# Optimization experiments

Hardware: AMD Instinct MI355X
Metric: run time of the kernel (lower is better)

## Reference

```python
import jax, jax.numpy as jnp
import numpy as np

N = 131072   # total nodes
G = 4096     # graphs
E = 524288   # directed bond edges
C = 96       # hidden_channels
L = 8        # num_layers
F_IN = 64    # atom features
NT = 5       # targets


def setup_inputs() -> dict:
    key = jax.random.key(0)
    ks = jax.random.split(key, 32)
    def rn(k, shape, s=0.05):
        return jax.random.normal(k, shape, jnp.float32) * s
    inp = {
        'x': jax.random.normal(ks[0], (N, F_IN), jnp.float32),
        'edge_index': jax.random.randint(ks[1], (2, E), 0, N),
        'batch': jnp.sort(jax.random.randint(ks[2], (N,), 0, G)),
        'num_graphs': G,
        # atom encoder
        'enc_w': rn(ks[3], (F_IN, C)), 'enc_b': rn(ks[4], (C,)),
        # virtual node embedding + MLP (Linear->BN->SiLU->Linear)
        'vn_emb': rn(ks[5], (C,)),
        'vn_w1': rn(ks[6], (C, C)), 'vn_b1': rn(ks[7], (C,)),
        'vn_g1': 1.0 + rn(ks[8], (C,)), 'vn_be1': rn(ks[9], (C,)),
        'vn_w2': rn(ks[10], (C, C)), 'vn_b2': rn(ks[11], (C,)),
        # per-layer GIN MLP (Linear C->2C, BN, SiLU, Linear 2C->C) stacked over L
        'conv_w1': rn(ks[12], (L, C, 2 * C)), 'conv_b1': rn(ks[13], (L, 2 * C)),
        'conv_g1': 1.0 + rn(ks[14], (L, 2 * C)), 'conv_be1': rn(ks[15], (L, 2 * C)),
        'conv_w2': rn(ks[16], (L, 2 * C, C)), 'conv_b2': rn(ks[17], (L, C)),
        # per-layer outer BatchNorm
        'bn_g': 1.0 + rn(ks[18], (L, C)), 'bn_b': rn(ks[19], (L, C)),
        # head: C->C/2 (BN,SiLU) -> C/4 (BN,SiLU) -> NT
        'h_w1': rn(ks[20], (C, C // 2)), 'h_b1': rn(ks[21], (C // 2,)),
        'h_g1': 1.0 + rn(ks[22], (C // 2,)), 'h_be1': rn(ks[23], (C // 2,)),
        'h_w2': rn(ks[24], (C // 2, C // 4)), 'h_b2': rn(ks[25], (C // 4,)),
        'h_g2': 1.0 + rn(ks[26], (C // 4,)), 'h_be2': rn(ks[27], (C // 4,)),
        'h_w3': rn(ks[28], (C // 4, NT)), 'h_b3': rn(ks[29], (NT,)),
    }
    return inp


def _bn(x, g, b, eps=1e-5):
    # training-mode BatchNorm1d: biased batch variance (matches torch normalization)
    m = x.mean(0)
    v = x.var(0)
    return (x - m) * jax.lax.rsqrt(v + eps) * g + b


def reference(x, edge_index, batch, num_graphs, enc_w, enc_b, vn_emb,
              vn_w1, vn_b1, vn_g1, vn_be1, vn_w2, vn_b2,
              conv_w1, conv_b1, conv_g1, conv_be1, conv_w2, conv_b2,
              bn_g, bn_b,
              h_w1, h_b1, h_g1, h_be1, h_w2, h_b2, h_g2, h_be2, h_w3, h_b3):
    n = x.shape[0]
    gN = int(num_graphs)
    c = enc_w.shape[1]
    nl = conv_w1.shape[0]

    h = x @ enc_w + enc_b                                   # [n, C]
    vn = jnp.broadcast_to(vn_emb, (gN, c))                  # virtual node feats
    h = jnp.concatenate([h, vn], 0)                         # [n+gN, C]

    # vectorized virtual-node edges: (n+batch[i]) <-> i, both directions
    node_ids = jnp.arange(n, dtype=batch.dtype)
    vidx = n + batch
    src = jnp.concatenate([edge_index[0], vidx, node_ids])
    tgt = jnp.concatenate([edge_index[1], node_ids, vidx])
    total = n + gN

    for i in range(nl):
        # GINConv, eps=0: MLP(x + sum_neighbors)
        agg = jax.ops.segment_sum(h[src], tgt, num_segments=total)
        z = h + agg
        z = z @ conv_w1[i] + conv_b1[i]
        z = jax.nn.silu(_bn(z, conv_g1[i], conv_be1[i]))
        z = z @ conv_w2[i] + conv_b2[i]
        z = jax.nn.silu(_bn(z, bn_g[i], bn_b[i]))           # outer BN + SiLU (dropout=eval)
        h = z if i == 0 else h + z                          # residual after layer 0
        if i < nl - 1:
            v = h[n:]
            v = jax.nn.silu(_bn(v @ vn_w1 + vn_b1, vn_g1, vn_be1)) @ vn_w2 + vn_b2
            h = jnp.concatenate([h[:n], v], 0)

    hn = h[:n]
    sums = jax.ops.segment_sum(hn, batch, num_segments=gN)
    counts = jax.ops.segment_sum(jnp.ones((n,), hn.dtype), batch, num_segments=gN)
    pooled = sums / jnp.maximum(counts, 1.0)[:, None]       # global_mean_pool

    z = jax.nn.silu(_bn(pooled @ h_w1 + h_b1, h_g1, h_be1))
    z = jax.nn.silu(_bn(z @ h_w2 + h_b2, h_g2, h_be2))
    return z @ h_w3 + h_b3                                  # [G, 5]
```

## Files before the change

kernel.cpp:

```cpp
#include <hip/hip_runtime.h>
#include <hip/hip_bf16.h>

constexpr int N_   = 131072;
constexpr int G_   = 4096;
constexpr int E_   = 524288;
constexpr int C_   = 96;
constexpr int L_   = 8;
constexpr int FIN_ = 64;
constexpr int TOT_ = N_ + G_;

typedef __attribute__((ext_vector_type(8))) short short8v;
typedef __attribute__((ext_vector_type(4))) float f32x4;
using bf16 = __hip_bfloat16;

__device__ __forceinline__ float silu_f(float y) { return y / (1.f + __expf(-y)); }
__device__ __forceinline__ float toF(float x) { return x; }
__device__ __forceinline__ float toF(bf16 x)  { return __bfloat162float(x); }
__device__ __forceinline__ float bfbits2f(short s) {
  return __uint_as_float(((unsigned)(unsigned short)s) << 16);
}
__device__ __forceinline__ short f2bfbits(float f) {
  bf16 b = __float2bfloat16(f);
  return *reinterpret_cast<short*>(&b);
}
__device__ __forceinline__ void atomAddD(double* p, double v) { unsafeAtomicAdd(p, v); }

static inline int gblk(long n) { return (int)((n + 255) / 256); }

__global__ __launch_bounds__(256) void k_prep(const float* __restrict__ enc_w,
    const float* __restrict__ conv_w1, const float* __restrict__ conv_w2,
    const float* __restrict__ vn_w1, const float* __restrict__ vn_w2,
    bf16* __restrict__ encwT, bf16* __restrict__ w1T, bf16* __restrict__ w2T,
    bf16* __restrict__ vnw1T, bf16* __restrict__ vnw2T) {
  int idx = blockIdx.x * 256 + threadIdx.x;
  const float* src; bf16* dst; int Kd, Nd, local;
  if (idx < 6144)        { src = enc_w;   dst = encwT; Kd = 64;  Nd = 96;  local = idx; }
  else if (idx < 153600) { src = conv_w1; dst = w1T;   Kd = 96;  Nd = 192; local = idx - 6144; }
  else if (idx < 301056) { src = conv_w2; dst = w2T;   Kd = 192; Nd = 96;  local = idx - 153600; }
  else if (idx < 310272) { src = vn_w1;   dst = vnw1T; Kd = 96;  Nd = 96;  local = idx - 301056; }
  else if (idx < 319488) { src = vn_w2;   dst = vnw2T; Kd = 96;  Nd = 96;  local = idx - 310272; }
  else return;
  int per = Kd * Nd;
  int i   = local / per;
  int rem = local - i * per;
  int k   = rem / Nd;
  int n   = rem - k * Nd;
  dst[(size_t)i * per + n * Kd + k] = __float2bfloat16(src[local]);
}

__global__ __launch_bounds__(256) void k_deg_count(const int* __restrict__ tgt, int* __restrict__ deg) {
  int e = blockIdx.x * 256 + threadIdx.x;
  if (e >= E_) return;
  atomicAdd(&deg[tgt[e]], 1);
}

__global__ __launch_bounds__(256) void k_scan_local(const int* __restrict__ deg, int* __restrict__ lp,
                                                    int* __restrict__ bsum) {
  __shared__ int s[256];
  int t = threadIdx.x;
  int i = blockIdx.x * 256 + t;
  int v = deg[i];
  s[t] = v;
  __syncthreads();
  for (int off = 1; off < 256; off <<= 1) {
    int x = (t >= off) ? s[t - off] : 0;
    __syncthreads();
    s[t] += x;
    __syncthreads();
  }
  lp[i] = s[t] - v;
  if (t == 255) bsum[blockIdx.x] = s[255];
}

__global__ __launch_bounds__(512) void k_scan_bsum(const int* __restrict__ bsum, int* __restrict__ boff) {
  __shared__ int s[512];
  int t = threadIdx.x;
  int v = bsum[t];
  s[t] = v;
  __syncthreads();
  for (int off = 1; off < 512; off <<= 1) {
    int x = (t >= off) ? s[t - off] : 0;
    __syncthreads();
    s[t] += x;
    __syncthreads();
  }
  boff[t] = s[t] - v;
}

__global__ __launch_bounds__(256) void k_scan_add(int* __restrict__ rs, const int* __restrict__ boff) {
  int i = blockIdx.x * 256 + threadIdx.x;
  if (i > N_) return;
  if (i == N_) { rs[N_] = E_; return; }
  rs[i] += boff[i >> 8];
}

__global__ __launch_bounds__(256) void k_csr_fill(const int* __restrict__ src, const int* __restrict__ tgt,
                                                  const int* __restrict__ rs, int* __restrict__ cur,
                                                  int* __restrict__ ssrc) {
  int e = blockIdx.x * 256 + threadIdx.x;
  if (e >= E_) return;
  int t = tgt[e];
  int pos = atomicAdd(&cur[t], 1);
  ssrc[rs[t] + pos] = src[e];
}

__global__ __launch_bounds__(256) void k_gbounds(const int* __restrict__ batch, int* __restrict__ gstart) {
  int i = blockIdx.x * 256 + threadIdx.x;
  if (i > N_) return;
  if (i == N_) {
    int last = batch[N_ - 1];
    for (int g = last + 1; g <= G_; ++g) gstart[g] = N_;
    return;
  }
  int b  = batch[i];
  int bp = (i == 0) ? -1 : batch[i - 1];
  for (int g = bp + 1; g <= b; ++g) gstart[g] = i;
}

__global__ __launch_bounds__(192) void k_vnagg(const bf16* __restrict__ hb, const int* __restrict__ gstart,
                                               bf16* __restrict__ vna) {
  int slot = threadIdx.x / 24;
  int c4   = (threadIdx.x % 24) * 4;
  int g = blockIdx.x * 8 + slot;
  int i0 = gstart[g], i1 = gstart[g + 1];
  float s0 = 0.f, s1 = 0.f, s2 = 0.f, s3 = 0.f;
  for (int i = i0; i < i1; ++i) {
    short4 v = *(const short4*)((const short*)hb + (size_t)i * C_ + c4);
    s0 += bfbits2f(v.x); s1 += bfbits2f(v.y); s2 += bfbits2f(v.z); s3 += bfbits2f(v.w);
  }
  short4 o;
  o.x = f2bfbits(s0); o.y = f2bfbits(s1); o.z = f2bfbits(s2); o.w = f2bfbits(s3);
  *(short4*)((short*)vna + (size_t)g * C_ + c4) = o;
}

template <int K, int NOUT, bool INACT, bool OSTATS, bool AF32, bool NTA, bool NTO, typename OutT>
__global__ __launch_bounds__(512) void k_gemm(const void* __restrict__ Aptr, const bf16* __restrict__ Wt,
                                              const float* __restrict__ bias,
                                              const double* __restrict__ stin,
                                              const float* __restrict__ gam, const float* __restrict__ bet,
                                              float Rin,
                                              OutT* __restrict__ out, double* __restrict__ stout) {
  constexpr int KK  = K / 32;
  constexpr int NT  = NOUT / 16;
  constexpr int UPR = K / 8;
  constexpr int LPR = UPR + 1;
  constexpr int LWB  = NOUT * LPR * 16;
  constexpr int ISCB = INACT ? 2 * K * 4 : 0;
  constexpr int SMB  = LWB + (ISCB > 0 ? ISCB : 1);
  __shared__ __align__(16) char smem[SMB];
  uint4* lw   = reinterpret_cast<uint4*>(smem);
  float* lsc  = reinterpret_cast<float*>(smem + LWB);
  float* lsh  = lsc + K;
  float* ssum = reinterpret_cast<float*>(smem);
  float* sqs  = ssum + 8 * NOUT;

  const uint4* wv = (const uint4*)Wt;
  for (int u = threadIdx.x; u < NOUT * UPR; u += 512) {
    int row = u / UPR, colu = u - row * UPR;
    lw[row * LPR + colu] = wv[u];
  }
  if (INACT) {
    for (int k = threadIdx.x; k < K; k += 512) {
      double mean = stin[k] / (double)Rin;
      double var  = stin[K + k] / (double)Rin - mean * mean;
      float sc = gam[k] * rsqrtf((float)var + 1e-5f);
      lsc[k] = sc;
      lsh[k] = bet[k] - (float)mean * sc;
    }
  }

  int wave = threadIdx.x >> 6, lane = threadIdx.x & 63;
  int m0 = (blockIdx.x * 8 + wave) * 16;
  int lr = lane & 15, lg = lane >> 4;

  short8v a[KK];
  if constexpr (AF32) {
    const float* Arow = (const float*)Aptr + (size_t)(m0 + lr) * K + lg * 8;
#pragma unroll
    for (int kk = 0; kk < KK; ++kk) {
      float4 f0 = *(const float4*)(Arow + kk * 32);
      float4 f1 = *(const float4*)(Arow + kk * 32 + 4);
      a[kk][0] = f2bfbits(f0.x); a[kk][1] = f2bfbits(f0.y);
      a[kk][2] = f2bfbits(f0.z); a[kk][3] = f2bfbits(f0.w);
      a[kk][4] = f2bfbits(f1.x); a[kk][5] = f2bfbits(f1.y);
      a[kk][6] = f2bfbits(f1.z); a[kk][7] = f2bfbits(f1.w);
    }
  } else {
    const short* Arow = (const short*)Aptr + (size_t)(m0 + lr) * K + lg * 8;
#pragma unroll
    for (int kk = 0; kk < KK; ++kk) {
      if constexpr (NTA) a[kk] = __builtin_nontemporal_load((const short8v*)(Arow + kk * 32));
      else               a[kk] = *(const short8v*)(Arow + kk * 32);
    }
  }

  __syncthreads();

  if (INACT) {
#pragma unroll
    for (int kk = 0; kk < KK; ++kk) {
      int kbase = kk * 32 + lg * 8;
#pragma unroll
      for (int j = 0; j < 8; ++j) {
        float f = bfbits2f(a[kk][j]);
        f = silu_f(fmaf(f, lsc[kbase + j], lsh[kbase + j]));
        a[kk][j] = f2bfbits(f);
      }
    }
  }

  f32x4 acc[NT];
#pragma unroll
  for (int nt = 0; nt < NT; ++nt) acc[nt] = (f32x4){0.f, 0.f, 0.f, 0.f};

#pragma unroll
  for (int nt = 0; nt < NT; ++nt) {
    const short* brow = (const short*)&lw[(nt * 16 + lr) * LPR] + lg * 8;
#pragma unroll
    for (int kk = 0; kk < KK; ++kk) {
      short8v b = *(const short8v*)(brow + kk * 32);
      acc[nt] = __builtin_amdgcn_mfma_f32_16x16x32_bf16(a[kk], b, acc[nt], 0, 0, 0);
    }
  }

  if (OSTATS) __syncthreads();

  int orow = m0 + (lg << 2);
#pragma unroll
  for (int nt = 0; nt < NT; ++nt) {
    int col = nt * 16 + lr;
    float bi = bias[col];
    float s = 0.f, q = 0.f;
#pragma unroll
    for (int r = 0; r < 4; ++r) {
      float y = acc[nt][r] + bi;
      float yb;
      size_t off = (size_t)(orow + r) * NOUT + col;
      if constexpr (sizeof(OutT) == 2) {
        short bits = f2bfbits(y);
        if constexpr (NTO) __builtin_nontemporal_store(bits, (short*)out + off);
        else               ((short*)out)[off] = bits;
        yb = bfbits2f(bits);
      } else {
        if constexpr (NTO) __builtin_nontemporal_store(y, (float*)out + off);
        else               ((float*)out)[off] = y;
        yb = y;
      }
      if (OSTATS) { s += yb; q += yb * yb; }
    }
    if (OSTATS) {
      s += __shfl_xor(s, 16, 64); s += __shfl_xor(s, 32, 64);
      q += __shfl_xor(q, 16, 64); q += __shfl_xor(q, 32, 64);
      if (lg == 0) { ssum[wave * NOUT + col] = s; sqs[wave * NOUT + col] = q; }
    }
  }
  if (OSTATS) {
    __syncthreads();
    int tid = threadIdx.x;
    if (tid < NOUT) {
      float s = 0.f, q = 0.f;
#pragma unroll
      for (int w = 0; w < 8; ++w) { s += ssum[w * NOUT + tid]; q += sqs[w * NOUT + tid]; }
      atomAddD(&stout[tid], (double)s);
      atomAddD(&stout[NOUT + tid], (double)q);
    }
  }
}

template <int K, int NOUT>
__global__ __launch_bounds__(512) void k_gemm_agg(const bf16* __restrict__ hb,
    const int* __restrict__ batch, const int* __restrict__ rs, const int* __restrict__ ssrc,
    const bf16* __restrict__ vna, const bf16* __restrict__ Wt, const float* __restrict__ bias,
    bf16* __restrict__ out, double* __restrict__ st) {
  constexpr int KK  = K / 32;
  constexpr int NT  = NOUT / 16;
  constexpr int UPR = K / 8;
  constexpr int LPR = UPR + 1;
  constexpr int LWB = NOUT * LPR * 16;
  __shared__ __align__(16) char smem[LWB];
  uint4* lw   = reinterpret_cast<uint4*>(smem);
  float* ssum = reinterpret_cast<float*>(smem);
  float* sqs  = ssum + 8 * NOUT;

  const uint4* wv = (const uint4*)Wt;
  for (int u = threadIdx.x; u < NOUT * UPR; u += 512) {
    int row = u / UPR, colu = u - row * UPR;
    lw[row * LPR + colu] = wv[u];
  }

  int wave = threadIdx.x >> 6, lane = threadIdx.x & 63;
  int m0 = (blockIdx.x * 8 + wave) * 16;
  int lr = lane & 15, lg = lane >> 4;
  int row = m0 + lr;
  int koff = lg * 8;

  float av[KK * 8];
#pragma unroll
  for (int t = 0; t < KK * 8; ++t) av[t] = 0.f;

  auto addPtr = [&](const short* p) {
#pragma unroll
    for (int kk = 0; kk < KK; ++kk) {
      short8v v = *(const short8v*)(p + koff + kk * 32);
#pragma unroll
      for (int j = 0; j < 8; ++j) av[kk * 8 + j] += bfbits2f(v[j]);
    }
  };
  auto addPtr2 = [&](const short* p0, const short* p1) {
    short8v v0[KK], v1[KK];
#pragma unroll
    for (int kk = 0; kk < KK; ++kk) {
      v0[kk] = *(const short8v*)(p0 + koff + kk * 32);
      v1[kk] = *(const short8v*)(p1 + koff + kk * 32);
    }
#pragma unroll
    for (int kk = 0; kk < KK; ++kk)
#pragma unroll
      for (int j = 0; j < 8; ++j)
        av[kk * 8 + j] += bfbits2f(v0[kk][j]) + bfbits2f(v1[kk][j]);
  };
  auto hrow = [&](int r) { return (const short*)hb + (size_t)r * K; };

  if (row < N_) {
    addPtr2(hrow(row), hrow(N_ + batch[row]));
    int e = rs[row], e1 = rs[row + 1];
    for (; e + 2 <= e1; e += 2) addPtr2(hrow(ssrc[e]), hrow(ssrc[e + 1]));
    if (e < e1) addPtr(hrow(ssrc[e]));
  } else {
    addPtr2(hrow(row), (const short*)vna + (size_t)(row - N_) * K);
  }

  short8v a[KK];
#pragma unroll
  for (int kk = 0; kk < KK; ++kk)
#pragma unroll
    for (int j = 0; j < 8; ++j) a[kk][j] = f2bfbits(av[kk * 8 + j]);

  __syncthreads();

  f32x4 acc[NT];
#pragma unroll
  for (int nt = 0; nt < NT; ++nt) acc[nt] = (f32x4){0.f, 0.f, 0.f, 0.f};

#pragma unroll
  for (int nt = 0; nt < NT; ++nt) {
    const short* brow = (const short*)&lw[(nt * 16 + lr) * LPR] + lg * 8;
#pragma unroll
    for (int kk = 0; kk < KK; ++kk) {
      short8v b = *(const short8v*)(brow + kk * 32);
      acc[nt] = __builtin_amdgcn_mfma_f32_16x16x32_bf16(a[kk], b, acc[nt], 0, 0, 0);
    }
  }

  __syncthreads();

  int orow = m0 + (lg << 2);
#pragma unroll
  for (int nt = 0; nt < NT; ++nt) {
    int col = nt * 16 + lr;
    float bi = bias[col];
    float s = 0.f, q = 0.f;
#pragma unroll
    for (int r = 0; r < 4; ++r) {
      float y = acc[nt][r] + bi;
      short bits = f2bfbits(y);
      __builtin_nontemporal_store(bits, (short*)out + (size_t)(orow + r) * NOUT + col);
      float yb = bfbits2f(bits);
      s += yb; q += yb * yb;
    }
    s += __shfl_xor(s, 16, 64); s += __shfl_xor(s, 32, 64);
    q += __shfl_xor(q, 16, 64); q += __shfl_xor(q, 32, 64);
    if (lg == 0) { ssum[wave * NOUT + col] = s; sqs[wave * NOUT + col] = q; }
  }
  __syncthreads();
  int tid = threadIdx.x;
  if (tid < NOUT) {
    float s = 0.f, q = 0.f;
#pragma unroll
    for (int w = 0; w < 8; ++w) { s += ssum[w * NOUT + tid]; q += sqs[w * NOUT + tid]; }
    atomAddD(&st[tid], (double)s);
    atomAddD(&st[NOUT + tid], (double)q);
  }
}

__global__ __launch_bounds__(256) void k_fill_vn(bf16* __restrict__ hb, const float* __restrict__ vn) {
  int idx = blockIdx.x * 256 + threadIdx.x;
  if (idx >= G_ * C_) return;
  int c = idx % C_;
  hb[(size_t)N_ * C_ + idx] = __float2bfloat16(vn[c]);
}

template <int CC, typename T>
__global__ __launch_bounds__(256) void k_bnstats(const T* __restrict__ X, int R, double* __restrict__ st) {
  int c = threadIdx.x;
  float s = 0.f, q = 0.f;
  for (int r = blockIdx.x; r < R; r += gridDim.x) {
    float v = toF(X[(size_t)r * CC + c]);
    s += v;
    q += v * v;
  }
  atomAddD(&st[c], (double)s);
  atomAddD(&st[CC + c], (double)q);
}

template <int CC>
__global__ __launch_bounds__(256) void k_bnfin(const double* __restrict__ st, int R,
    const float* __restrict__ g, const float* __restrict__ be,
    float* __restrict__ scale, float* __restrict__ shift) {
  int c = threadIdx.x;
  if (c >= CC) return;
  double mean = st[c] / R;
  double var  = st[CC + c] / R - mean * mean;
  float sc = g[c] * rsqrtf((float)var + 1e-5f);
  scale[c] = sc;
  shift[c] = be[c] - (float)mean * sc;
}

__global__ __launch_bounds__(256) void k_update(const bf16* __restrict__ Z, bf16* __restrict__ hb,
    const double* __restrict__ st,
    const float* __restrict__ gam, const float* __restrict__ bet, int addResid) {
  __shared__ float lsc[C_], lsh[C_];
  if (threadIdx.x < C_) {
    int c = threadIdx.x;
    double mean = st[c] / (double)TOT_;
    double var  = st[C_ + c] / (double)TOT_ - mean * mean;
    float sc = gam[c] * rsqrtf((float)var + 1e-5f);
    lsc[c] = sc;
    lsh[c] = bet[c] - (float)mean * sc;
  }
  __syncthreads();
  int idx = blockIdx.x * 256 + threadIdx.x;
  if (idx >= TOT_ * C_ / 8) return;
  int cg = idx % (C_ / 8);
  int c0 = cg * 8;
  short8v zv = __builtin_nontemporal_load((const short8v*)Z + idx);
  short8v hv = ((const short8v*)hb)[idx];
  short8v o;
#pragma unroll
  for (int j = 0; j < 8; ++j) {
    float y = silu_f(fmaf(bfbits2f(zv[j]), lsc[c0 + j], lsh[c0 + j]));
    float hn = addResid ? (bfbits2f(hv[j]) + y) : y;
    o[j] = f2bfbits(hn);
  }
  ((short8v*)hb)[idx] = o;
}

template <int K, int M, bool INACT>
__global__ __launch_bounds__(256) void k_mm(const float* __restrict__ A,
    const float* __restrict__ W, const float* __restrict__ bias,
    const float* __restrict__ isc, const float* __restrict__ ish,
    float* __restrict__ out, int R) {
  int idx = blockIdx.x * 256 + threadIdx.x;
  if (idx >= R * M) return;
  int row = idx / M;
  int m   = idx - row * M;
  const float* ar = A + (size_t)row * K;
  float s = bias[m];
#pragma unroll 8
  for (int k = 0; k < K; ++k) {
    float a = ar[k];
    if (INACT) a = silu_f(fmaf(a, isc[k], ish[k]));
    s = fmaf(a, W[k * M + m], s);
  }
  out[idx] = s;
}

__global__ __launch_bounds__(256) void k_pool2(const bf16* __restrict__ hb, const int* __restrict__ gstart,
                                               float* __restrict__ pooled) {
  int idx = blockIdx.x * 256 + threadIdx.x;
  if (idx >= G_ * C_) return;
  int g = idx / C_;
  int c = idx - g * C_;
  int i0 = gstart[g], i1 = gstart[g + 1];
  float s = 0.f;
  for (int i = i0; i < i1; ++i) s += toF(hb[(size_t)i * C_ + c]);
  pooled[idx] = s / fmaxf((float)(i1 - i0), 1.0f);
}

extern "C" void kernel_launch(void* const* d_in, const int* in_sizes, int n_in,
                              void* d_out, int out_size, void* d_ws, size_t ws_size,
                              hipStream_t stream) {
  (void)in_sizes; (void)n_in; (void)out_size; (void)ws_size;
  const float* x       = (const float*)d_in[0];
  const int*   ei      = (const int*)d_in[1];
  const int*   batch   = (const int*)d_in[2];
  const float* enc_w   = (const float*)d_in[4];
  const float* enc_b   = (const float*)d_in[5];
  const float* vn_emb  = (const float*)d_in[6];
  const float* vn_w1   = (const float*)d_in[7];
  const float* vn_b1   = (const float*)d_in[8];
  const float* vn_g1   = (const float*)d_in[9];
  const float* vn_be1  = (const float*)d_in[10];
  const float* vn_w2   = (const float*)d_in[11];
  const float* vn_b2   = (const float*)d_in[12];
  const float* conv_w1 = (const float*)d_in[13];
  const float* conv_b1 = (const float*)d_in[14];
  const float* conv_g1 = (const float*)d_in[15];
  const float* conv_be1= (const float*)d_in[16];
  const float* conv_w2 = (const float*)d_in[17];
  const float* conv_b2 = (const float*)d_in[18];
  const float* bn_g    = (const float*)d_in[19];
  const float* bn_b    = (const float*)d_in[20];
  const float* h_w1    = (const float*)d_in[21];
  const float* h_b1    = (const float*)d_in[22];
  const float* h_g1    = (const float*)d_in[23];
  const float* h_be1   = (const float*)d_in[24];
  const float* h_w2    = (const float*)d_in[25];
  const float* h_b2    = (const float*)d_in[26];
  const float* h_g2    = (const float*)d_in[27];
  const float* h_be2   = (const float*)d_in[28];
  const float* h_w3    = (const float*)d_in[29];
  const float* h_b3    = (const float*)d_in[30];
  float* out = (float*)d_out;

  const int* e_src = ei;
  const int* e_tgt = ei + E_;

  char* p = (char*)d_ws;
  auto alloc = [&](size_t bytes) -> char* {
    char* r = p;
    p += (bytes + 15) & ~size_t(15);
    return r;
  };
  bf16*   hbf    = (bf16*)  alloc((size_t)TOT_ * C_ * 2);
  bf16*   vna    = (bf16*)  alloc((size_t)G_ * C_ * 2);
  bf16*   vtb    = (bf16*)  alloc((size_t)G_ * C_ * 2);
  float*  pooled = (float*) alloc((size_t)G_ * C_ * 4);
  float*  t1     = (float*) alloc((size_t)G_ * 48 * 4);
  float*  t2     = (float*) alloc((size_t)G_ * 24 * 4);
  float*  scale1 = (float*) alloc(256 * 4);
  float*  shift1 = (float*) alloc(256 * 4);
  float*  scale2 = (float*) alloc(256 * 4);
  float*  shift2 = (float*) alloc(256 * 4);
  double* stbuf  = (double*)alloc((size_t)26 * 384 * 8);
  bf16*   z1     = (bf16*)  alloc((size_t)TOT_ * 2 * C_ * 2);
  bf16*   z2     = (bf16*)  alloc((size_t)TOT_ * C_ * 2);
  bf16*   encwT  = (bf16*)  alloc((size_t)C_ * FIN_ * 2);
  bf16*   w1T    = (bf16*)  alloc((size_t)L_ * 2 * C_ * C_ * 2);
  bf16*   w2T    = (bf16*)  alloc((size_t)L_ * C_ * 2 * C_ * 2);
  bf16*   vnw1T  = (bf16*)  alloc((size_t)C_ * C_ * 2);
  bf16*   vnw2T  = (bf16*)  alloc((size_t)C_ * C_ * 2);
  int*    deg    = (int*)   alloc((size_t)N_ * 4);
  int*    cur    = (int*)   alloc((size_t)N_ * 4);
  int*    rs     = (int*)   alloc((size_t)(N_ + 1) * 4);
  int*    bsum   = (int*)   alloc(512 * 4);
  int*    boff   = (int*)   alloc(512 * 4);
  int*    ssrc   = (int*)   alloc((size_t)E_ * 4);
  int*    gstart = (int*)   alloc((size_t)(G_ + 1) * 4);

  auto ST = [&](int i) { return stbuf + (size_t)i * 384; };

  k_prep<<<gblk(319488), 256, 0, stream>>>(enc_w, conv_w1, conv_w2, vn_w1, vn_w2,
                                           encwT, w1T, w2T, vnw1T, vnw2T);

  hipMemsetAsync(deg, 0, (size_t)N_ * 4, stream);
  hipMemsetAsync(cur, 0, (size_t)N_ * 4, stream);
  hipMemsetAsync(stbuf, 0, (size_t)26 * 384 * 8, stream);
  k_deg_count<<<gblk(E_), 256, 0, stream>>>(e_tgt, deg);
  k_scan_local<<<N_ / 256, 256, 0, stream>>>(deg, rs, bsum);
  k_scan_bsum<<<1, 512, 0, stream>>>(bsum, boff);
  k_scan_add<<<gblk(N_ + 1), 256, 0, stream>>>(rs, boff);
  k_csr_fill<<<gblk(E_), 256, 0, stream>>>(e_src, e_tgt, rs, cur, ssrc);
  k_gbounds<<<gblk(N_ + 1), 256, 0, stream>>>(batch, gstart);

  k_gemm<FIN_, C_, false, false, true, false, false, bf16><<<N_ / 128, 512, 0, stream>>>(
      x, encwT, enc_b, nullptr, nullptr, nullptr, 1.f, hbf, nullptr);
  k_fill_vn<<<gblk((long)G_ * C_), 256, 0, stream>>>(hbf, vn_emb);

  for (int i = 0; i < L_; ++i) {
    const bf16*  wt1 = w1T + (size_t)i * 2 * C_ * C_;
    const bf16*  wt2 = w2T + (size_t)i * C_ * 2 * C_;
    const float* b1  = conv_b1 + (size_t)i * 2 * C_;
    const float* g1  = conv_g1 + (size_t)i * 2 * C_;
    const float* be1 = conv_be1+ (size_t)i * 2 * C_;
    const float* b2  = conv_b2 + (size_t)i * C_;
    const float* bg  = bn_g    + (size_t)i * C_;
    const float* bb  = bn_b    + (size_t)i * C_;

    k_vnagg<<<G_ / 8, 192, 0, stream>>>(hbf, gstart, vna);

    k_gemm_agg<C_, 2 * C_><<<TOT_ / 128, 512, 0, stream>>>(
        hbf, batch, rs, ssrc, vna, wt1, b1, z1, ST(i));

    k_gemm<2 * C_, C_, true, true, false, true, true, bf16><<<TOT_ / 128, 512, 0, stream>>>(
        z1, wt2, b2, ST(i), g1, be1, (float)TOT_, z2, ST(8 + i));

    k_update<<<(int)((long)TOT_ * C_ / 8 / 256), 256, 0, stream>>>(z2, hbf, ST(8 + i), bg, bb, i > 0);

    if (i < L_ - 1) {
      k_gemm<C_, C_, false, true, false, false, false, bf16><<<G_ / 128, 512, 0, stream>>>(
          hbf + (size_t)N_ * C_, vnw1T, vn_b1, nullptr, nullptr, nullptr, 1.f, vtb, ST(16 + i));
      k_gemm<C_, C_, true, false, false, false, false, bf16><<<G_ / 128, 512, 0, stream>>>(
          vtb, vnw2T, vn_b2, ST(16 + i), vn_g1, vn_be1, (float)G_,
          hbf + (size_t)N_ * C_, nullptr);
    }
  }

  k_pool2<<<gblk((long)G_ * C_), 256, 0, stream>>>(hbf, gstart, pooled);

  k_mm<C_, 48, false><<<gblk((long)G_ * 48), 256, 0, stream>>>(
      pooled, h_w1, h_b1, nullptr, nullptr, t1, G_);
  k_bnstats<48, float><<<64, 48, 0, stream>>>(t1, G_, ST(23));
  k_bnfin<48><<<1, 48, 0, stream>>>(ST(23), G_, h_g1, h_be1, scale1, shift1);

  k_mm<48, 24, true><<<gblk((long)G_ * 24), 256, 0, stream>>>(
      t1, h_w2, h_b2, scale1, shift1, t2, G_);
  k_bnstats<24, float><<<64, 24, 0, stream>>>(t2, G_, ST(24));
  k_bnfin<24><<<1, 24, 0, stream>>>(ST(24), G_, h_g2, h_be2, scale2, shift2);

  k_mm<24, 5, true><<<gblk((long)G_ * 5), 256, 0, stream>>>(
      t2, h_w3, h_b3, scale2, shift2, out, G_);
}
```

Before: 1.440 ms.

## Sort nodes by degree for load-balanced aggregation; drop nontemporal loads/stores

Builds a degree-bucketed permutation of nodes (histogram, prefix base, scatter) once per call, and has the aggregation+GEMM kernel process rows in that order so lanes within a wave walk similar neighbor counts, reducing divergence. Output rows are scattered back through the permutation via shuffled row ids. Also removes the nontemporal load/store variants from the GEMM, aggregation and update kernels so these intermediates can stay in cache. The price is extra setup kernels, an indirection per row, and scattered output writes.

```diff
diff --git a/kernel.cpp b/kernel.cpp
--- a/kernel.cpp
+++ b/kernel.cpp
@@ -117,6 +117,29 @@
   for (int g = bp + 1; g <= b; ++g) gstart[g] = i;
 }
 
+__global__ __launch_bounds__(256) void k_deghist(const int* __restrict__ deg, int* __restrict__ hist) {
+  int i = blockIdx.x * 256 + threadIdx.x;
+  if (i >= N_) return;
+  int b = deg[i]; if (b > 32) b = 32;
+  atomicAdd(&hist[b], 1);
+}
+
+__global__ __launch_bounds__(64) void k_degbase(const int* __restrict__ hist, int* __restrict__ base) {
+  if (threadIdx.x == 0) {
+    int acc = 0;
+    for (int b = 0; b < 33; ++b) { base[b] = acc; acc += hist[b]; }
+  }
+}
+
+__global__ __launch_bounds__(256) void k_permfill(const int* __restrict__ deg, const int* __restrict__ base,
+                                                  int* __restrict__ curs, int* __restrict__ perm) {
+  int i = blockIdx.x * 256 + threadIdx.x;
+  if (i >= N_) return;
+  int b = deg[i]; if (b > 32) b = 32;
+  int pos = atomicAdd(&curs[b], 1);
+  perm[base[b] + pos] = i;
+}
+
 __global__ __launch_bounds__(192) void k_vnagg(const bf16* __restrict__ hb, const int* __restrict__ gstart,
                                                bf16* __restrict__ vna) {
   int slot = threadIdx.x / 24;
@@ -133,7 +156,7 @@
   *(short4*)((short*)vna + (size_t)g * C_ + c4) = o;
 }
 
-template <int K, int NOUT, bool INACT, bool OSTATS, bool AF32, bool NTA, bool NTO, typename OutT>
+template <int K, int NOUT, bool INACT, bool OSTATS, bool AF32, typename OutT>
 __global__ __launch_bounds__(512) void k_gemm(const void* __restrict__ Aptr, const bf16* __restrict__ Wt,
                                               const float* __restrict__ bias,
                                               const double* __restrict__ stin,
@@ -188,10 +211,7 @@
   } else {
     const short* Arow = (const short*)Aptr + (size_t)(m0 + lr) * K + lg * 8;
 #pragma unroll
-    for (int kk = 0; kk < KK; ++kk) {
-      if constexpr (NTA) a[kk] = __builtin_nontemporal_load((const short8v*)(Arow + kk * 32));
-      else               a[kk] = *(const short8v*)(Arow + kk * 32);
-    }
+    for (int kk = 0; kk < KK; ++kk) a[kk] = *(const short8v*)(Arow + kk * 32);
   }
 
   __syncthreads();
@@ -238,12 +258,10 @@
       size_t off = (size_t)(orow + r) * NOUT + col;
       if constexpr (sizeof(OutT) == 2) {
         short bits = f2bfbits(y);
-        if constexpr (NTO) __builtin_nontemporal_store(bits, (short*)out + off);
-        else               ((short*)out)[off] = bits;
+        ((short*)out)[off] = bits;
         yb = bfbits2f(bits);
       } else {
-        if constexpr (NTO) __builtin_nontemporal_store(y, (float*)out + off);
-        else               ((float*)out)[off] = y;
+        ((float*)out)[off] = y;
         yb = y;
       }
       if (OSTATS) { s += yb; q += yb * yb; }
@@ -270,7 +288,8 @@
 template <int K, int NOUT>
 __global__ __launch_bounds__(512) void k_gemm_agg(const bf16* __restrict__ hb,
     const int* __restrict__ batch, const int* __restrict__ rs, const int* __restrict__ ssrc,
-    const bf16* __restrict__ vna, const bf16* __restrict__ Wt, const float* __restrict__ bias,
+    const bf16* __restrict__ vna, const int* __restrict__ perm,
+    const bf16* __restrict__ Wt, const float* __restrict__ bias,
     bf16* __restrict__ out, double* __restrict__ st) {
   constexpr int KK  = K / 32;
   constexpr int NT  = NOUT / 16;
@@ -292,6 +311,7 @@
   int m0 = (blockIdx.x * 8 + wave) * 16;
   int lr = lane & 15, lg = lane >> 4;
   int row = m0 + lr;
+  int rowo = (m0 < N_) ? perm[row] : row;
   int koff = lg * 8;
 
   float av[KK * 8];
@@ -321,13 +341,13 @@
   };
   auto hrow = [&](int r) { return (const short*)hb + (size_t)r * K; };
 
-  if (row < N_) {
-    addPtr2(hrow(row), hrow(N_ + batch[row]));
-    int e = rs[row], e1 = rs[row + 1];
+  if (m0 < N_) {
+    addPtr2(hrow(rowo), hrow(N_ + batch[rowo]));
+    int e = rs[rowo], e1 = rs[rowo + 1];
     for (; e + 2 <= e1; e += 2) addPtr2(hrow(ssrc[e]), hrow(ssrc[e + 1]));
     if (e < e1) addPtr(hrow(ssrc[e]));
   } else {
-    addPtr2(hrow(row), (const short*)vna + (size_t)(row - N_) * K);
+    addPtr2(hrow(rowo), (const short*)vna + (size_t)(rowo - N_) * K);
   }
 
   short8v a[KK];
@@ -354,7 +374,10 @@
 
   __syncthreads();
 
-  int orow = m0 + (lg << 2);
+  int rid[4];
+#pragma unroll
+  for (int r = 0; r < 4; ++r) rid[r] = __shfl(rowo, (lg << 2) + r, 64);
+
 #pragma unroll
   for (int nt = 0; nt < NT; ++nt) {
     int col = nt * 16 + lr;
@@ -364,7 +387,7 @@
     for (int r = 0; r < 4; ++r) {
       float y = acc[nt][r] + bi;
       short bits = f2bfbits(y);
-      __builtin_nontemporal_store(bits, (short*)out + (size_t)(orow + r) * NOUT + col);
+      ((short*)out)[(size_t)rid[r] * NOUT + col] = bits;
       float yb = bfbits2f(bits);
       s += yb; q += yb * yb;
     }
@@ -433,7 +456,7 @@
   if (idx >= TOT_ * C_ / 8) return;
   int cg = idx % (C_ / 8);
   int c0 = cg * 8;
-  short8v zv = __builtin_nontemporal_load((const short8v*)Z + idx);
+  short8v zv = ((const short8v*)Z)[idx];
   short8v hv = ((const short8v*)hb)[idx];
   short8v o;
 #pragma unroll
@@ -547,6 +570,10 @@
   int*    boff   = (int*)   alloc(512 * 4);
   int*    ssrc   = (int*)   alloc((size_t)E_ * 4);
   int*    gstart = (int*)   alloc((size_t)(G_ + 1) * 4);
+  int*    perm   = (int*)   alloc((size_t)N_ * 4);
+  int*    hist   = (int*)   alloc(33 * 4);
+  int*    hbase  = (int*)   alloc(33 * 4);
+  int*    hcurs  = (int*)   alloc(33 * 4);
 
   auto ST = [&](int i) { return stbuf + (size_t)i * 384; };
 
@@ -556,14 +583,19 @@
   hipMemsetAsync(deg, 0, (size_t)N_ * 4, stream);
   hipMemsetAsync(cur, 0, (size_t)N_ * 4, stream);
   hipMemsetAsync(stbuf, 0, (size_t)26 * 384 * 8, stream);
+  hipMemsetAsync(hist, 0, 33 * 4, stream);
+  hipMemsetAsync(hcurs, 0, 33 * 4, stream);
   k_deg_count<<<gblk(E_), 256, 0, stream>>>(e_tgt, deg);
   k_scan_local<<<N_ / 256, 256, 0, stream>>>(deg, rs, bsum);
   k_scan_bsum<<<1, 512, 0, stream>>>(bsum, boff);
   k_scan_add<<<gblk(N_ + 1), 256, 0, stream>>>(rs, boff);
   k_csr_fill<<<gblk(E_), 256, 0, stream>>>(e_src, e_tgt, rs, cur, ssrc);
   k_gbounds<<<gblk(N_ + 1), 256, 0, stream>>>(batch, gstart);
-
-  k_gemm<FIN_, C_, false, false, true, false, false, bf16><<<N_ / 128, 512, 0, stream>>>(
+  k_deghist<<<gblk(N_), 256, 0, stream>>>(deg, hist);
+  k_degbase<<<1, 64, 0, stream>>>(hist, hbase);
+  k_permfill<<<gblk(N_), 256, 0, stream>>>(deg, hbase, hcurs, perm);
+
+  k_gemm<FIN_, C_, false, false, true, bf16><<<N_ / 128, 512, 0, stream>>>(
       x, encwT, enc_b, nullptr, nullptr, nullptr, 1.f, hbf, nullptr);
   k_fill_vn<<<gblk((long)G_ * C_), 256, 0, stream>>>(hbf, vn_emb);
 
@@ -580,17 +612,17 @@
     k_vnagg<<<G_ / 8, 192, 0, stream>>>(hbf, gstart, vna);
 
     k_gemm_agg<C_, 2 * C_><<<TOT_ / 128, 512, 0, stream>>>(
-        hbf, batch, rs, ssrc, vna, wt1, b1, z1, ST(i));
-
-    k_gemm<2 * C_, C_, true, true, false, true, true, bf16><<<TOT_ / 128, 512, 0, stream>>>(
+        hbf, batch, rs, ssrc, vna, perm, wt1, b1, z1, ST(i));
+
+    k_gemm<2 * C_, C_, true, true, false, bf16><<<TOT_ / 128, 512, 0, stream>>>(
         z1, wt2, b2, ST(i), g1, be1, (float)TOT_, z2, ST(8 + i));
 
     k_update<<<(int)((long)TOT_ * C_ / 8 / 256), 256, 0, stream>>>(z2, hbf, ST(8 + i), bg, bb, i > 0);
 
     if (i < L_ - 1) {
-      k_gemm<C_, C_, false, true, false, false, false, bf16><<<G_ / 128, 512, 0, stream>>>(
+      k_gemm<C_, C_, false, true, false, bf16><<<G_ / 128, 512, 0, stream>>>(
           hbf + (size_t)N_ * C_, vnw1T, vn_b1, nullptr, nullptr, nullptr, 1.f, vtb, ST(16 + i));
-      k_gemm<C_, C_, true, false, false, false, false, bf16><<<G_ / 128, 512, 0, stream>>>(
+      k_gemm<C_, C_, true, false, false, bf16><<<G_ / 128, 512, 0, stream>>>(
           vtb, vnw2T, vn_b2, ST(16 + i), vn_g1, vn_be1, (float)G_,
           hbf + (size_t)N_ * C_, nullptr);
     }
```

After: 2.341 ms. 1.63x slower.
